# Kernel optimization log

Hardware: AMD Instinct MI355X
Metric: run time of the kernel (lower is better)

The kernel has to match this reference:

```python
import jax, jax.numpy as jnp
import numpy as np

# Sizes: B graphs of N nodes each, K nearest neighbours, D=feat_dim=nhid, C=pos_dim
B, N, K, D, C = 4, 1024, 128, 32, 2
L = 3                     # number of EGNN conv layers
E_IN = 2 * D + 1          # edge MLP input: feats_i | feats_j | rel_dist (edge_dim=0, fourier=0)
E_H = 2 * E_IN            # edge MLP hidden


def _lin(key, fan_in, fan_out):
    kw, kb = jax.random.split(key)
    w = jax.random.normal(kw, (fan_in, fan_out), jnp.float32) / np.sqrt(fan_in)
    b = jax.random.normal(kb, (fan_out,), jnp.float32) * 0.01
    return w, b


def _stack(key, fan_in, fan_out):
    ws, bs = zip(*[_lin(k, fan_in, fan_out) for k in jax.random.split(key, L)])
    return jnp.stack(ws), jnp.stack(bs)


def setup_inputs() -> dict:
    key = jax.random.key(0)
    ks = jax.random.split(key, 10)
    feat_ = jax.random.normal(ks[0], (B * N, D), jnp.float32)
    coor_ = jax.random.normal(ks[1], (B * N, C), jnp.float32)
    batch = jnp.full((B,), N, dtype=jnp.int32)   # per-graph node counts (equal-size graphs)
    embed_w, embed_b = _lin(ks[2], D, D)         # embed: Linear(feat_dim, nhid)
    e1_w, e1_b = _stack(ks[3], E_IN, E_H)        # edge MLP
    e2_w, e2_b = _stack(ks[4], E_H, D)           # -> m_dim = nhid
    gate_w, gate_b = _stack(ks[5], D, 1)         # soft_edges gate
    c1_w, c1_b = _stack(ks[6], D, 4 * D)         # coors MLP
    c2_w, c2_b = _stack(ks[7], 4 * D, 1)
    n1_w, n1_b = _stack(ks[8], 2 * D, 2 * D)     # node MLP
    n2_w, n2_b = _stack(ks[9], 2 * D, D)
    coors_scale = jnp.full((L, 1), 1e-2, jnp.float32)  # CoorsNorm scale (init 1e-2)
    return dict(feat_=feat_, coor_=coor_, batch=batch, embed_w=embed_w, embed_b=embed_b,
                e1_w=e1_w, e1_b=e1_b, e2_w=e2_w, e2_b=e2_b, gate_w=gate_w, gate_b=gate_b,
                c1_w=c1_w, c1_b=c1_b, c2_w=c2_w, c2_b=c2_b, n1_w=n1_w, n1_b=n1_b,
                n2_w=n2_w, n2_b=n2_b, coors_scale=coors_scale)


def _lrelu(x):
    return jax.nn.leaky_relu(x, 0.1)


def _gather(x, idx):
    # x: [B, n, d], idx: [B, n, k] -> [B, n, k, d]
    return jax.vmap(lambda xb, ib: xb[ib])(x, idx)


def _egnn_layer(feats, coors, p):
    (e1_w, e1_b, e2_w, e2_b, gate_w, gate_b, c1_w, c1_b, c2_w, c2_b,
     n1_w, n1_b, n2_w, n2_b, scale) = p
    # pairwise squared distances; k smallest (self included, valid_radius=inf)
    diff = coors[:, :, None, :] - coors[:, None, :, :]      # [B,n,n,C]
    dist = jnp.sum(diff * diff, axis=-1)                    # [B,n,n]
    neg_d, idx = jax.lax.top_k(-dist, K)                    # k nearest
    rel_dist = -neg_d[..., None]                            # [B,n,K,1]
    rel_coors = coors[:, :, None, :] - _gather(coors, idx)  # [B,n,K,C]
    feats_j = _gather(feats, idx)                           # [B,n,K,D]
    feats_i = jnp.broadcast_to(feats[:, :, None, :], feats_j.shape)
    edge_in = jnp.concatenate([feats_i, feats_j, rel_dist], axis=-1)  # [B,n,K,E_IN]
    # edge MLP: Lin -> act -> Lin -> act ; soft edge gate
    m = _lrelu(_lrelu(edge_in @ e1_w + e1_b) @ e2_w + e2_b)            # [B,n,K,D]
    m = m * jax.nn.sigmoid(m @ gate_w + gate_b)
    # coordinate update: coors_mlp -> scalar weights; CoorsNorm on rel coords
    cw = (_lrelu(m @ c1_w + c1_b) @ c2_w + c2_b)[..., 0]               # [B,n,K]
    norm = jnp.maximum(jnp.linalg.norm(rel_coors, axis=-1, keepdims=True), 1e-8)
    rel_n = rel_coors / norm * scale
    coors_out = jnp.einsum('bik,bikc->bic', cw, rel_n) + coors
    # feature update: sum-pool messages, node MLP with residual
    m_i = jnp.sum(m, axis=2)                                           # [B,n,D]
    node_in = jnp.concatenate([feats, m_i], axis=-1)
    feats_out = _lrelu(node_in @ n1_w + n1_b) @ n2_w + n2_b + feats
    return feats_out, coors_out


def reference(feat_, coor_, batch, embed_w, embed_b, e1_w, e1_b, e2_w, e2_b,
              gate_w, gate_b, c1_w, c1_b, c2_w, c2_b, n1_w, n1_b, n2_w, n2_b,
              coors_scale):
    # embed MLP (dropout is identity at p=0 / eval), then batch equal-size graphs
    feats = _lrelu(feat_ @ embed_w + embed_b).reshape(B, N, D)
    coors = coor_.reshape(B, N, C)
    for l in range(L):
        p = (e1_w[l], e1_b[l], e2_w[l], e2_b[l], gate_w[l], gate_b[l],
             c1_w[l], c1_b[l], c2_w[l], c2_b[l], n1_w[l], n1_b[l],
             n2_w[l], n2_b[l], coors_scale[l])
        feats, coors = _egnn_layer(feats, coors, p)
    return feats.reshape(B * N, D)
```

## Files before the change

kernel.cpp:

```cpp
#include <hip/hip_runtime.h>
#include <hip/hip_bf16.h>
#include <math.h>

#define BB 4
#define NN 1024
#define KK 128
#define DD 32
#define LL 3
#define EH 130
#define EHP 132

typedef float f32x4 __attribute__((ext_vector_type(4)));
typedef short s16x8 __attribute__((ext_vector_type(8)));

__device__ __forceinline__ float lrelu(float x) { return fmaxf(x, 0.1f * x); }

__device__ __forceinline__ unsigned pk2(float a, float b) {
    __hip_bfloat162 h = __float22bfloat162_rn(float2{a, b});
    return *(unsigned*)&h;
}
__device__ __forceinline__ unsigned short bf16_hu(float v) {
    return (unsigned short)((__float_as_uint(v) + 0x8000u) >> 16);
}
__device__ __forceinline__ unsigned short bf16_rne(float v) {
    unsigned u = __float_as_uint(v);
    return (unsigned short)((u + 0x7fffu + ((u >> 16) & 1u)) >> 16);
}

__global__ __launch_bounds__(256) void prep_kernel(
    const float* __restrict__ feat, const float* __restrict__ ew, const float* __restrict__ eb,
    float* __restrict__ out,
    const float* __restrict__ e2w, const float* __restrict__ c1w,
    unsigned short* __restrict__ e2f, unsigned short* __restrict__ c1f) {
    if (blockIdx.x < 512) {
        int t = blockIdx.x * 256 + threadIdx.x;
        if (t >= BB * NN * DD) return;
        int n = t >> 5, o = t & 31;
        const float* f = feat + n * DD;
        float a = eb[o];
#pragma unroll
        for (int k = 0; k < DD; k++) a = fmaf(f[k], ew[k * DD + o], a);
        out[t] = lrelu(a);
    } else {
        int t = (blockIdx.x - 512) * 256 + threadIdx.x;
        if (t < LL * 4 * 2 * 512) {
            int jj = t & 7, lane = (t >> 3) & 63, nt = (t >> 9) & 1, c = (t >> 10) & 3, l = t >> 12;
            int k = 32 * c + (lane >> 4) * 8 + jj;
            int n = nt * 16 + (lane & 15);
            e2f[t] = bf16_rne(e2w[(size_t)l * EH * DD + k * DD + n]);
        } else {
            int u = t - LL * 4 * 2 * 512;
            if (u < LL * 8 * 512) {
                int jj = u & 7, lane = (u >> 3) & 63, nt = (u >> 9) & 7, l = u >> 12;
                int k = (lane >> 4) * 8 + jj;
                int n = nt * 16 + (lane & 15);
                c1f[u] = bf16_rne(c1w[(size_t)l * DD * 128 + k * 128 + n]);
            }
        }
    }
}

__global__ __launch_bounds__(256) void knnpre_kernel(
    const float* __restrict__ coors, int* __restrict__ nbr,
    const float* __restrict__ feats, const float* __restrict__ e1w, const float* __restrict__ e1b,
    float* __restrict__ HI, float* __restrict__ HJ) {
    if (blockIdx.x >= BB * NN) {
        int t = (int)(blockIdx.x - BB * NN) * 256 + threadIdx.x;
        if (t >= BB * NN * EHP) return;
        int n = t / EHP, o = t % EHP;
        if (o >= EH) { HI[t] = 0.f; HJ[t] = 0.f; return; }
        const float* f = feats + n * DD;
        float a = e1b[o], c = 0.f;
#pragma unroll
        for (int k = 0; k < DD; k++) a = fmaf(f[k], e1w[k * EH + o], a);
#pragma unroll
        for (int k = 0; k < DD; k++) c = fmaf(f[k], e1w[(DD + k) * EH + o], c);
        HI[t] = a;
        HJ[t] = c;
        return;
    }
    const int node = blockIdx.x;
    const int b = node >> 10, i = node & (NN - 1);
    const int t = threadIdx.x;
    const int lane = t & 63, w = t >> 6;

    __shared__ unsigned cand[NN];
    __shared__ unsigned hh[256];
    __shared__ unsigned wsum[4];
    __shared__ unsigned bsel[3];
    __shared__ unsigned scnt[3];
    __shared__ unsigned sdstar;

    const float2* cb = (const float2*)(coors + (size_t)b * NN * 2);
    const float2 ci = cb[i];
    unsigned k4[4];
#pragma unroll
    for (int c = 0; c < 4; c++) {
        int j = t + c * 256;
        float2 cj = cb[j];
        float dx = ci.x - cj.x, dy = ci.y - cj.y;
        float d = __fadd_rn(__fmul_rn(dx, dx), __fmul_rn(dy, dy));
        k4[c] = __float_as_uint(d);
    }
    if (t < 3) scnt[t] = 0;

    unsigned maskSo = 0u, valSo = 0u;
    unsigned R = KK - 1;
    unsigned c = NN;
    for (int pass = 0; pass < 4 && c > 256u; pass++) {
        const int shift = 24 - 8 * pass;
        hh[t] = 0;
        __syncthreads();
#pragma unroll
        for (int cc = 0; cc < 4; cc++) {
            unsigned k = k4[cc];
            if ((k & maskSo) == valSo) atomicAdd(&hh[(k >> shift) & 255u], 1u);
        }
        __syncthreads();
        const unsigned mine = hh[t];
        unsigned v = mine;
#pragma unroll
        for (int off = 1; off < 64; off <<= 1) {
            unsigned u = __shfl_up(v, off, 64);
            if (lane >= off) v += u;
        }
        if (lane == 63) wsum[w] = v;
        __syncthreads();
        unsigned pre = 0;
#pragma unroll
        for (int s = 0; s < 3; s++) if (s < w) pre += wsum[s];
        const unsigned cum = v + pre;
        if (R < cum && R >= cum - mine) { bsel[0] = (unsigned)t; bsel[1] = cum - mine; bsel[2] = mine; }
        __syncthreads();
        valSo |= bsel[0] << shift;
        maskSo |= 255u << shift;
        R -= bsel[1];
        c = bsel[2];
        __syncthreads();
    }

    unsigned dstar;
    if (c > 256u) {
        dstar = valSo;
    } else {
#pragma unroll
        for (int cc = 0; cc < 4; cc++) {
            unsigned k = k4[cc];
            if ((k & maskSo) == valSo) {
                unsigned slot = atomicAdd(&scnt[2], 1u);
                cand[slot] = k;
            }
        }
        __syncthreads();
        if (t < (int)c) {
            const unsigned kt = cand[t];
            unsigned less = 0, eq = 0;
            for (unsigned s = 0; s < c; s++) {
                unsigned ks = cand[s];
                less += (ks < kt);
                eq += (ks == kt);
            }
            if (less <= R && R < less + eq) sdstar = kt;
        }
        __syncthreads();
        dstar = sdstar;
    }

#pragma unroll
    for (int cc = 0; cc < 4; cc++) {
        int j = t + cc * 256;
        unsigned k = k4[cc];
        if (k < dstar) {
            unsigned slot = atomicAdd(&scnt[0], 1u);
            nbr[(size_t)node * KK + slot] = j;
        } else if (k == dstar) {
            unsigned slot = atomicAdd(&scnt[1], 1u);
            cand[slot] = (unsigned)j;
        }
    }
    __syncthreads();
    const unsigned base = scnt[0];
    const int E = (int)scnt[1];
    const int need = KK - (int)base;
    if (E == need) {
        for (int cc = t; cc < E; cc += 256)
            nbr[(size_t)node * KK + base + cc] = (int)cand[cc];
    } else {
        for (int r = 0; r < need; r++) {
            unsigned best = 0xFFFFFFFFu;
            for (int cc = t; cc < E; cc += 256) best = min(best, cand[cc]);
            hh[t] = best;
            __syncthreads();
            for (int off = 128; off >= 1; off >>= 1) {
                if (t < off) hh[t] = min(hh[t], hh[t + off]);
                __syncthreads();
            }
            unsigned win = hh[0];
            __syncthreads();
            if (t == 0) nbr[(size_t)node * KK + base + r] = (int)win;
            for (int cc = t; cc < E; cc += 256)
                if (cand[cc] == win) cand[cc] = 0xFFFFFFFFu;
            __syncthreads();
        }
    }
}

__global__ __launch_bounds__(128) void layer_kernel(
    const float* __restrict__ feats_in, const float* __restrict__ coors_in,
    const int*   __restrict__ nbr,
    const float* __restrict__ HI, const float* __restrict__ HJ,
    const float* __restrict__ w65,
    const float* __restrict__ e2w,
    const float* __restrict__ e2b,
    const unsigned short* __restrict__ e2f,
    const unsigned short* __restrict__ c1f,
    const float* __restrict__ gw, const float* __restrict__ gb,
    const float* __restrict__ c1b, const float* __restrict__ c2w, const float* __restrict__ c2b,
    const float* __restrict__ n1w, const float* __restrict__ n1b,
    const float* __restrict__ n2w, const float* __restrict__ n2b,
    const float* __restrict__ scale,
    float* __restrict__ feats_out, float* __restrict__ coors_out) {
    const int node = blockIdx.x;
    const int b = node >> 10;
    const int t = threadIdx.x;
    const int lane = t & 63, wid = t >> 6;
    const int ln = lane & 15, q = lane >> 4;
    const int rowbase = wid * 64;

    __shared__ __align__(16) float shi[EHP];
    __shared__ __align__(16) float sw65[EHP];
    __shared__ __align__(16) unsigned short smA[2 * 64 * 32];
    __shared__ float sx0[128], sx1[128], su[128], sv[128];
    __shared__ float sgw[DD], se2b[DD], sfi[DD];
    __shared__ float sc1b[128], sc2w[128];
    __shared__ float redm[2][DD], redc[2][2];
    __shared__ float sni[2 * DD], shd[2 * DD];

    for (int u = t; u < EHP; u += 128) {
        shi[u] = HI[(size_t)node * EHP + u];
        sw65[u] = (u < EH) ? w65[u] : 0.f;
    }
    if (t < DD) { sfi[t] = feats_in[node * DD + t]; sgw[t] = gw[t]; se2b[t] = e2b[t]; }
    sc1b[t] = c1b[t];
    sc2w[t] = c2w[t];
    __syncthreads();

    const float cix = coors_in[node * 2], ciy = coors_in[node * 2 + 1];
    const int j = nbr[(size_t)node * KK + t];
    const float2 cj = *(const float2*)(coors_in + ((size_t)(b * NN) + j) * 2);
    const float dx = cix - cj.x, dy = ciy - cj.y;
    const float rd = __fadd_rn(__fmul_rn(dx, dx), __fmul_rn(dy, dy));
    const float nrm = fmaxf(sqrtf(rd), 1e-8f);
    const float s = scale[0] / nrm;
    su[t] = dx * s;
    sv[t] = dy * s;

    {
        const float2 hjt = *(const float2*)(HJ + ((size_t)(b * NN) + j) * EHP + 128);
        sx0[t] = lrelu(shi[128] + hjt.x + rd * sw65[128]);
        sx1[t] = lrelu(shi[129] + hjt.y + rd * sw65[129]);
    }

    const float* hjb[4];
    float rdR[4];
#pragma unroll
    for (int mt = 0; mt < 4; mt++) {
        int jR = __shfl(j, mt * 16 + ln, 64);
        rdR[mt] = __shfl(rd, mt * 16 + ln, 64);
        hjb[mt] = HJ + ((size_t)(b * NN) + jR) * EHP;
    }

    const float4* shi4 = (const float4*)shi;
    const float4* sw4  = (const float4*)sw65;

    const f32x4 zz = {0.f, 0.f, 0.f, 0.f};
    f32x4 accA[4][2];
#pragma unroll
    for (int mt = 0; mt < 4; mt++) { accA[mt][0] = zz; accA[mt][1] = zz; }

#pragma unroll 1
    for (int c = 0; c < 4; c++) {
        s16x8 b0 = *(const s16x8*)(e2f + ((c * 2 + 0) * 64 + lane) * 8);
        s16x8 b1 = *(const s16x8*)(e2f + ((c * 2 + 1) * 64 + lane) * 8);
        const int kb = c * 8 + q * 2;
        const float4 hi0 = shi4[kb], hi1 = shi4[kb + 1];
        const float4 wv0 = sw4[kb],  wv1 = sw4[kb + 1];
#pragma unroll
        for (int mt = 0; mt < 4; mt++) {
            const float4* hjp = (const float4*)(hjb[mt] + c * 32 + q * 8);
            const float4 ha = hjp[0], hb = hjp[1];
            const float r = rdR[mt];
            union { s16x8 v; unsigned u[4]; } A;
            A.u[0] = pk2(lrelu(hi0.x + ha.x + r * wv0.x), lrelu(hi0.y + ha.y + r * wv0.y));
            A.u[1] = pk2(lrelu(hi0.z + ha.z + r * wv0.z), lrelu(hi0.w + ha.w + r * wv0.w));
            A.u[2] = pk2(lrelu(hi1.x + hb.x + r * wv1.x), lrelu(hi1.y + hb.y + r * wv1.y));
            A.u[3] = pk2(lrelu(hi1.z + hb.z + r * wv1.z), lrelu(hi1.w + hb.w + r * wv1.w));
            accA[mt][0] = __builtin_amdgcn_mfma_f32_16x16x32_bf16(A.v, b0, accA[mt][0], 0, 0, 0);
            accA[mt][1] = __builtin_amdgcn_mfma_f32_16x16x32_bf16(A.v, b1, accA[mt][1], 0, 0, 0);
        }
    }

#pragma unroll
    for (int nt = 0; nt < 2; nt++) {
        const int col = nt * 16 + ln;
        const float w128 = e2w[128 * DD + col];
        const float w129 = e2w[129 * DD + col];
        const float bv = se2b[col];
#pragma unroll
        for (int mt = 0; mt < 4; mt++)
#pragma unroll
            for (int r = 0; r < 4; r++) {
                const int row = rowbase + mt * 16 + q * 4 + r;
                accA[mt][nt][r] = lrelu(accA[mt][nt][r] + bv + sx0[row] * w128 + sx1[row] * w129);
            }
    }

    const float gbv = gb[0];
#pragma unroll
    for (int mt = 0; mt < 4; mt++) {
        float p[4];
#pragma unroll
        for (int r = 0; r < 4; r++)
            p[r] = accA[mt][0][r] * sgw[ln] + accA[mt][1][r] * sgw[16 + ln];
#pragma unroll
        for (int off = 1; off <= 8; off <<= 1)
#pragma unroll
            for (int r = 0; r < 4; r++) p[r] += __shfl_xor(p[r], off);
#pragma unroll
        for (int r = 0; r < 4; r++) {
            const float g = 1.f / (1.f + __expf(-(p[r] + gbv)));
            accA[mt][0][r] *= g;
            accA[mt][1][r] *= g;
        }
    }

    float mi0 = 0.f, mi1 = 0.f;
#pragma unroll
    for (int mt = 0; mt < 4; mt++)
#pragma unroll
        for (int r = 0; r < 4; r++) { mi0 += accA[mt][0][r]; mi1 += accA[mt][1][r]; }
    mi0 += __shfl_xor(mi0, 16); mi0 += __shfl_xor(mi0, 32);
    mi1 += __shfl_xor(mi1, 16); mi1 += __shfl_xor(mi1, 32);
    if (lane < 16) { redm[wid][lane] = mi0; redm[wid][16 + lane] = mi1; }

    unsigned short* smw = smA + wid * (64 * 32);
#pragma unroll
    for (int mt = 0; mt < 4; mt++)
#pragma unroll
        for (int nt = 0; nt < 2; nt++)
#pragma unroll
            for (int r = 0; r < 4; r++) {
                const int prow = (r << 4) | (4 * mt + q);
                smw[prow * 32 + nt * 16 + ln] = bf16_hu(accA[mt][nt][r]);
            }

    s16x8 a4[4];
#pragma unroll
    for (int mt = 0; mt < 4; mt++) {
        const int prow = ((ln & 3) << 4) | (4 * mt + (ln >> 2));
        a4[mt] = *(const s16x8*)(smw + prow * 32 + q * 8);
    }

    float cacc[4][4];
#pragma unroll
    for (int mt = 0; mt < 4; mt++)
#pragma unroll
        for (int r = 0; r < 4; r++) cacc[mt][r] = 0.f;

#pragma unroll 1
    for (int g = 0; g < 4; g++) {
        s16x8 bc0 = *(const s16x8*)(c1f + ((2 * g + 0) * 64 + lane) * 8);
        s16x8 bc1 = *(const s16x8*)(c1f + ((2 * g + 1) * 64 + lane) * 8);
        f32x4 c20[4], c21[4];
#pragma unroll
        for (int mt = 0; mt < 4; mt++) {
            c20[mt] = __builtin_amdgcn_mfma_f32_16x16x32_bf16(a4[mt], bc0, zz, 0, 0, 0);
            c21[mt] = __builtin_amdgcn_mfma_f32_16x16x32_bf16(a4[mt], bc1, zz, 0, 0, 0);
        }
#pragma unroll
        for (int h = 0; h < 2; h++) {
            const int col = (2 * g + h) * 16 + ln;
            const float c1bv = sc1b[col], c2wv = sc2w[col];
#pragma unroll
            for (int mt = 0; mt < 4; mt++)
#pragma unroll
                for (int r = 0; r < 4; r++) {
                    const float v = (h ? c21[mt][r] : c20[mt][r]) + c1bv;
                    cacc[mt][r] = fmaf(lrelu(v), c2wv, cacc[mt][r]);
                }
        }
    }
#pragma unroll
    for (int off = 1; off <= 8; off <<= 1)
#pragma unroll
        for (int mt = 0; mt < 4; mt++)
#pragma unroll
            for (int r = 0; r < 4; r++) cacc[mt][r] += __shfl_xor(cacc[mt][r], off);

    const float c2bv = c2b[0];
    float vxp = 0.f, vyp = 0.f;
    if (ln == 0) {
#pragma unroll
        for (int mt = 0; mt < 4; mt++)
#pragma unroll
            for (int r = 0; r < 4; r++) {
                const int row = rowbase + mt * 16 + q * 4 + r;
                const float cw = cacc[mt][r] + c2bv;
                vxp = fmaf(cw, su[row], vxp);
                vyp = fmaf(cw, sv[row], vyp);
            }
    }
    vxp += __shfl_xor(vxp, 16); vxp += __shfl_xor(vxp, 32);
    vyp += __shfl_xor(vyp, 16); vyp += __shfl_xor(vyp, 32);
    if (lane == 0) { redc[wid][0] = vxp; redc[wid][1] = vyp; }

    __syncthreads();
    if (t < DD) {
        sni[t] = sfi[t];
        sni[DD + t] = redm[0][t] + redm[1][t];
    }
    __syncthreads();
    if (t < 2 * DD) {
        float a = n1b[t];
#pragma unroll
        for (int k = 0; k < 2 * DD; k++) a = fmaf(sni[k], n1w[k * 2 * DD + t], a);
        shd[t] = lrelu(a);
    }
    __syncthreads();
    if (t < DD) {
        float a = n2b[t];
#pragma unroll
        for (int o = 0; o < 2 * DD; o++) a = fmaf(shd[o], n2w[o * DD + t], a);
        feats_out[node * DD + t] = a + sfi[t];
    }
    if (t == 0) {
        coors_out[node * 2] = cix + redc[0][0] + redc[1][0];
        coors_out[node * 2 + 1] = ciy + redc[0][1] + redc[1][1];
    }
}

extern "C" void kernel_launch(void* const* d_in, const int* in_sizes, int n_in,
                              void* d_out, int out_size, void* d_ws, size_t ws_size,
                              hipStream_t stream) {
    const float* feat_   = (const float*)d_in[0];
    const float* coor_   = (const float*)d_in[1];
    const float* embed_w = (const float*)d_in[3];
    const float* embed_b = (const float*)d_in[4];
    const float* e1_w    = (const float*)d_in[5];
    const float* e1_b    = (const float*)d_in[6];
    const float* e2_w    = (const float*)d_in[7];
    const float* e2_b    = (const float*)d_in[8];
    const float* gate_w  = (const float*)d_in[9];
    const float* gate_b  = (const float*)d_in[10];
    const float* c1_w    = (const float*)d_in[11];
    const float* c1_b    = (const float*)d_in[12];
    const float* c2_w    = (const float*)d_in[13];
    const float* c2_b    = (const float*)d_in[14];
    const float* n1_w    = (const float*)d_in[15];
    const float* n1_b    = (const float*)d_in[16];
    const float* n2_w    = (const float*)d_in[17];
    const float* n2_b    = (const float*)d_in[18];
    const float* cscale  = (const float*)d_in[19];

    float* ws = (float*)d_ws;
    float* feats_a = ws;               ws += BB * NN * DD;
    float* feats_b = ws;               ws += BB * NN * DD;
    float* coors_a = ws;               ws += BB * NN * 2;
    float* coors_b = ws;               ws += BB * NN * 2;
    float* HI      = ws;               ws += BB * NN * EHP;
    float* HJ      = ws;               ws += BB * NN * EHP;
    unsigned short* e2f = (unsigned short*)ws;
    unsigned short* c1f = e2f + LL * 4096;
    ws += (2 * LL * 4096) / 2;
    int* nbr = (int*)ws;

    prep_kernel<<<512 + 96, 256, 0, stream>>>(feat_, embed_w, embed_b, feats_a,
                                              e2_w, c1_w, e2f, c1f);

    const int PREB = (BB * NN * EHP + 255) / 256;
    const float* fin = feats_a;
    const float* cin = coor_;
    float* fouts[LL] = {feats_b, feats_a, (float*)d_out};
    float* couts[LL] = {coors_a, coors_b, coors_a};

    for (int l = 0; l < LL; l++) {
        knnpre_kernel<<<BB * NN + PREB, 256, 0, stream>>>(
            cin, nbr, fin, e1_w + (size_t)l * 65 * EH, e1_b + (size_t)l * EH, HI, HJ);
        layer_kernel<<<BB * NN, 128, 0, stream>>>(
            fin, cin, nbr, HI, HJ,
            e1_w + ((size_t)l * 65 + 64) * EH,
            e2_w + (size_t)l * EH * DD,
            e2_b + (size_t)l * DD,
            e2f + (size_t)l * 4096,
            c1f + (size_t)l * 4096,
            gate_w + (size_t)l * DD,
            gate_b + l,
            c1_b + (size_t)l * 128,
            c2_w + (size_t)l * 128,
            c2_b + l,
            n1_w + (size_t)l * 64 * 64,
            n1_b + (size_t)l * 64,
            n2_w + (size_t)l * 64 * 32,
            n2_b + (size_t)l * DD,
            cscale + l,
            fouts[l], couts[l]);
        fin = fouts[l];
        cin = couts[l];
    }
}
```

Baseline: 384.1 us.

## Replace block-wide radix-select kNN with one-wavefront-per-node bitwise binary search

The kNN selection moves from one 256-thread block per node, which used a shared-memory radix histogram with many barriers, to one 64-lane wavefront per node. Each lane holds 16 distances in registers and finds the K-th smallest key by a 31-step bitwise binary search over counts reduced with shuffles. Neighbours are then written through a wavefront prefix scan, and ties are resolved by ballot in index order. This removes shared-memory atomics and __syncthreads and cuts the block count by four, at the cost of 31 serial count-and-reduce rounds per node.

```diff
diff --git a/kernel.cpp b/kernel.cpp
--- a/kernel.cpp
+++ b/kernel.cpp
@@ -64,8 +64,9 @@
     const float* __restrict__ coors, int* __restrict__ nbr,
     const float* __restrict__ feats, const float* __restrict__ e1w, const float* __restrict__ e1b,
     float* __restrict__ HI, float* __restrict__ HJ) {
-    if (blockIdx.x >= BB * NN) {
-        int t = (int)(blockIdx.x - BB * NN) * 256 + threadIdx.x;
+    const int KNNB = BB * NN / 4;
+    if (blockIdx.x >= KNNB) {
+        int t = (int)(blockIdx.x - KNNB) * 256 + threadIdx.x;
         if (t >= BB * NN * EHP) return;
         int n = t / EHP, o = t % EHP;
         if (o >= EH) { HI[t] = 0.f; HJ[t] = 0.f; return; }
@@ -79,129 +80,58 @@
         HJ[t] = c;
         return;
     }
-    const int node = blockIdx.x;
+    const int node = (int)blockIdx.x * 4 + (threadIdx.x >> 6);
     const int b = node >> 10, i = node & (NN - 1);
-    const int t = threadIdx.x;
-    const int lane = t & 63, w = t >> 6;
-
-    __shared__ unsigned cand[NN];
-    __shared__ unsigned hh[256];
-    __shared__ unsigned wsum[4];
-    __shared__ unsigned bsel[3];
-    __shared__ unsigned scnt[3];
-    __shared__ unsigned sdstar;
+    const int lane = threadIdx.x & 63;
 
     const float2* cb = (const float2*)(coors + (size_t)b * NN * 2);
     const float2 ci = cb[i];
-    unsigned k4[4];
-#pragma unroll
-    for (int c = 0; c < 4; c++) {
-        int j = t + c * 256;
-        float2 cj = cb[j];
+    unsigned k[16];
+#pragma unroll
+    for (int s = 0; s < 16; s++) {
+        float2 cj = cb[lane + 64 * s];
         float dx = ci.x - cj.x, dy = ci.y - cj.y;
         float d = __fadd_rn(__fmul_rn(dx, dx), __fmul_rn(dy, dy));
-        k4[c] = __float_as_uint(d);
-    }
-    if (t < 3) scnt[t] = 0;
-
-    unsigned maskSo = 0u, valSo = 0u;
-    unsigned R = KK - 1;
-    unsigned c = NN;
-    for (int pass = 0; pass < 4 && c > 256u; pass++) {
-        const int shift = 24 - 8 * pass;
-        hh[t] = 0;
-        __syncthreads();
-#pragma unroll
-        for (int cc = 0; cc < 4; cc++) {
-            unsigned k = k4[cc];
-            if ((k & maskSo) == valSo) atomicAdd(&hh[(k >> shift) & 255u], 1u);
-        }
-        __syncthreads();
-        const unsigned mine = hh[t];
-        unsigned v = mine;
-#pragma unroll
-        for (int off = 1; off < 64; off <<= 1) {
-            unsigned u = __shfl_up(v, off, 64);
-            if (lane >= off) v += u;
-        }
-        if (lane == 63) wsum[w] = v;
-        __syncthreads();
-        unsigned pre = 0;
-#pragma unroll
-        for (int s = 0; s < 3; s++) if (s < w) pre += wsum[s];
-        const unsigned cum = v + pre;
-        if (R < cum && R >= cum - mine) { bsel[0] = (unsigned)t; bsel[1] = cum - mine; bsel[2] = mine; }
-        __syncthreads();
-        valSo |= bsel[0] << shift;
-        maskSo |= 255u << shift;
-        R -= bsel[1];
-        c = bsel[2];
-        __syncthreads();
-    }
-
-    unsigned dstar;
-    if (c > 256u) {
-        dstar = valSo;
-    } else {
-#pragma unroll
-        for (int cc = 0; cc < 4; cc++) {
-            unsigned k = k4[cc];
-            if ((k & maskSo) == valSo) {
-                unsigned slot = atomicAdd(&scnt[2], 1u);
-                cand[slot] = k;
-            }
-        }
-        __syncthreads();
-        if (t < (int)c) {
-            const unsigned kt = cand[t];
-            unsigned less = 0, eq = 0;
-            for (unsigned s = 0; s < c; s++) {
-                unsigned ks = cand[s];
-                less += (ks < kt);
-                eq += (ks == kt);
-            }
-            if (less <= R && R < less + eq) sdstar = kt;
-        }
-        __syncthreads();
-        dstar = sdstar;
-    }
-
-#pragma unroll
-    for (int cc = 0; cc < 4; cc++) {
-        int j = t + cc * 256;
-        unsigned k = k4[cc];
-        if (k < dstar) {
-            unsigned slot = atomicAdd(&scnt[0], 1u);
-            nbr[(size_t)node * KK + slot] = j;
-        } else if (k == dstar) {
-            unsigned slot = atomicAdd(&scnt[1], 1u);
-            cand[slot] = (unsigned)j;
-        }
-    }
-    __syncthreads();
-    const unsigned base = scnt[0];
-    const int E = (int)scnt[1];
-    const int need = KK - (int)base;
-    if (E == need) {
-        for (int cc = t; cc < E; cc += 256)
-            nbr[(size_t)node * KK + base + cc] = (int)cand[cc];
-    } else {
-        for (int r = 0; r < need; r++) {
-            unsigned best = 0xFFFFFFFFu;
-            for (int cc = t; cc < E; cc += 256) best = min(best, cand[cc]);
-            hh[t] = best;
-            __syncthreads();
-            for (int off = 128; off >= 1; off >>= 1) {
-                if (t < off) hh[t] = min(hh[t], hh[t + off]);
-                __syncthreads();
-            }
-            unsigned win = hh[0];
-            __syncthreads();
-            if (t == 0) nbr[(size_t)node * KK + base + r] = (int)win;
-            for (int cc = t; cc < E; cc += 256)
-                if (cand[cc] == win) cand[cc] = 0xFFFFFFFFu;
-            __syncthreads();
-        }
+        k[s] = __float_as_uint(d);
+    }
+
+    unsigned P = 0;
+    for (int bpos = 30; bpos >= 0; bpos--) {
+        const unsigned X = P | (1u << bpos);
+        unsigned c = 0;
+#pragma unroll
+        for (int s = 0; s < 16; s++) c += (k[s] < X) ? 1u : 0u;
+#pragma unroll
+        for (int off = 1; off < 64; off <<= 1) c += __shfl_xor(c, off, 64);
+        if (c < (unsigned)KK) P = X;
+    }
+    const unsigned dstar = P;
+
+    unsigned myc = 0;
+#pragma unroll
+    for (int s = 0; s < 16; s++) myc += (k[s] < dstar) ? 1u : 0u;
+    unsigned inc = myc;
+#pragma unroll
+    for (int off = 1; off < 64; off <<= 1) {
+        unsigned u = __shfl_up(inc, off, 64);
+        if (lane >= off) inc += u;
+    }
+    unsigned pos = inc - myc;
+    const unsigned total_less = __shfl(inc, 63, 64);
+    int* nb = nbr + (size_t)node * KK;
+#pragma unroll
+    for (int s = 0; s < 16; s++)
+        if (k[s] < dstar) nb[pos++] = lane + 64 * s;
+
+    const int need = KK - (int)total_less;
+    unsigned tie_so_far = 0;
+    for (int s = 0; s < 16 && (int)tie_so_far < need; s++) {
+        unsigned long long mask = __ballot(k[s] == dstar);
+        if (k[s] == dstar) {
+            unsigned r = tie_so_far + (unsigned)__popcll(mask & ((1ull << lane) - 1ull));
+            if ((int)r < need) nb[total_less + r] = lane + 64 * s;
+        }
+        tie_so_far += (unsigned)__popcll(mask);
     }
 }
 
@@ -477,6 +407,7 @@
     prep_kernel<<<512 + 96, 256, 0, stream>>>(feat_, embed_w, embed_b, feats_a,
                                               e2_w, c1_w, e2f, c1f);
 
+    const int KNNB = BB * NN / 4;
     const int PREB = (BB * NN * EHP + 255) / 256;
     const float* fin = feats_a;
     const float* cin = coor_;
@@ -484,7 +415,7 @@
     float* couts[LL] = {coors_a, coors_b, coors_a};
 
     for (int l = 0; l < LL; l++) {
-        knnpre_kernel<<<BB * NN + PREB, 256, 0, stream>>>(
+        knnpre_kernel<<<KNNB + PREB, 256, 0, stream>>>(
             cin, nbr, fin, e1_w + (size_t)l * 65 * EH, e1_b + (size_t)l * EH, HI, HJ);
         layer_kernel<<<BB * NN, 128, 0, stream>>>(
             fin, cin, nbr, HI, HJ,
```

After: 362.3 us. 5.7% less time.
